# Kernel optimization log

Measured on AMD Instinct MI355X. Metric: run time of the kernel, lower is better.

The kernel has to match this reference:

```python
import jax, jax.numpy as jnp
import numpy as np

B = 1024        # graphs per batch
NPG = 64        # nodes per graph (uniform)
DEG = 16        # avg degree
NE_PG = 256     # candidate non-edges per graph
N = B * NPG
E = N * DEG
NE = B * NE_PG
EMB, HID, NCAT, NET, NOUT = 64, 128, 100, 4, 101  # NOUT = num_external + 1


def setup_inputs() -> dict:
    key = jax.random.key(0)
    ks = jax.random.split(key, 32)
    rn = lambda k, shape: jax.random.normal(k, shape, jnp.float32) * 0.05
    # graph structure: edges and non-edges stay within each graph's node block
    x = jax.random.randint(ks[0], (N,), 0, NCAT)
    offs = jnp.repeat(jnp.arange(B) * NPG, NPG * DEG)
    src = jax.random.randint(ks[1], (E,), 0, NPG) + offs
    dst = jax.random.randint(ks[2], (E,), 0, NPG) + offs
    edge_index = jnp.stack([src, dst])
    edge_attr = jax.random.randint(ks[3], (E,), 0, NET)
    offs_ne = jnp.repeat(jnp.arange(B) * NPG, NE_PG)
    non_edges = jax.random.randint(ks[4], (NE, 2), 0, NPG) + offs_ne[:, None]
    batch = jnp.repeat(jnp.arange(B), NPG)
    return dict(
        node_tab=rn(ks[5], (NCAT, EMB)), edge_tab=rn(ks[6], (NET, EMB)),
        c1_w=rn(ks[7], (EMB, HID)), c1_we=rn(ks[8], (EMB, HID)),
        c1_as=rn(ks[9], (HID,)), c1_ad=rn(ks[10], (HID,)), c1_ae=rn(ks[11], (HID,)), c1_b=rn(ks[12], (HID,)),
        c2_w=rn(ks[13], (HID, HID)), c2_we=rn(ks[14], (EMB, HID)),
        c2_as=rn(ks[15], (HID,)), c2_ad=rn(ks[16], (HID,)), c2_ae=rn(ks[17], (HID,)), c2_b=rn(ks[18], (HID,)),
        s_w1=rn(ks[19], (HID, HID)), s_b1=rn(ks[20], (HID,)), s_w2=rn(ks[21], (HID, 1)), s_b2=rn(ks[22], (1,)),
        n_w1=rn(ks[23], (HID, HID)), n_b1=rn(ks[24], (HID,)), n_w2=rn(ks[25], (HID, NOUT)), n_b2=rn(ks[26], (NOUT,)),
        e_w1=rn(ks[27], (HID, HID)), e_b1=rn(ks[28], (HID,)), e_w2=rn(ks[29], (HID, 1)), e_b2=rn(ks[30], (1,)),
        x=x, edge_index=edge_index, edge_attr=edge_attr, non_edges=non_edges, batch=batch,
    )


def _gat(h_in, src, dst, e, W, We, a_s, a_d, a_e, b):
    """PyG GATConv, heads=1: gather -> leakyrelu logits -> segment softmax over dst -> scatter sum."""
    n = h_in.shape[0]
    h = h_in @ W                  # [N, C]
    he = e @ We                   # [E, C]
    logit = (h @ a_s)[src] + (h @ a_d)[dst] + he @ a_e   # [E]
    logit = jnp.where(logit > 0, logit, 0.2 * logit)      # leaky_relu(0.2)
    m = jax.ops.segment_max(logit, dst, num_segments=n)
    ex = jnp.exp(logit - m[dst])
    den = jax.ops.segment_sum(ex, dst, num_segments=n)
    alpha = ex / (den[dst] + 1e-16)
    return jax.ops.segment_sum(h[src] * alpha[:, None], dst, num_segments=n) + b


def _mlp(z, w1, b1, w2, b2):
    return jax.nn.relu(z @ w1 + b1) @ w2 + b2


def reference(node_tab, edge_tab,
              c1_w, c1_we, c1_as, c1_ad, c1_ae, c1_b,
              c2_w, c2_we, c2_as, c2_ad, c2_ae, c2_b,
              s_w1, s_b1, s_w2, s_b2,
              n_w1, n_b1, n_w2, n_b2,
              e_w1, e_b1, e_w2, e_b2,
              x, edge_index, edge_attr, non_edges, batch):
    src, dst = edge_index[0], edge_index[1]
    e = edge_tab[edge_attr]                      # [E, EMB]
    h = node_tab[x]                              # [N, EMB]
    h = jax.nn.relu(_gat(h, src, dst, e, c1_w, c1_we, c1_as, c1_ad, c1_ae, c1_b))
    h = _gat(h, src, dst, e, c2_w, c2_we, c2_as, c2_ad, c2_ae, c2_b)   # [N, HID]
    g = jax.ops.segment_sum(h, batch, num_segments=B)                   # [B, HID]
    stop = _mlp(g, s_w1, s_b1, s_w2, s_b2)                              # [B, 1]
    addnode = _mlp(h, n_w1, n_b1, n_w2, n_b2)                           # [N, NOUT]
    pair = h[non_edges[:, 0]] + h[non_edges[:, 1]]                      # [NE, HID]
    addedge = _mlp(pair, e_w1, e_b1, e_w2, e_b2)                        # [NE, 1]
    # uniform per-graph sizes -> the torch split/pad is a static reshape+concat
    return jnp.concatenate(
        [stop, addnode.reshape(B, NPG * NOUT), addedge.reshape(B, NE_PG)], axis=1)
```

## Files before the change

kernel.cpp:

```cpp
#include <hip/hip_runtime.h>


#define NPG 64
#define EPG 1024
#define NEPG 256
#define B_GR 1024
#define E_TOT 1048576
#define EMB 64
#define HID 128
#define NOUT 101
#define OUT_PG 6721

typedef __attribute__((ext_vector_type(8))) short bf16x8;
typedef __attribute__((ext_vector_type(4))) float f32x4;
typedef unsigned short ushort_t;

__device__ ushort_t g_c1w[EMB*HID];
__device__ ushort_t g_c2w[HID*HID];
__device__ ushort_t g_nw1[HID*HID];
__device__ ushort_t g_ew1[HID*HID];
__device__ ushort_t g_nw2[HID*112];
__device__ float    g_sw1t[HID*HID];
__device__ float    g_he1[4], g_he2[4];

__device__ __forceinline__ ushort_t f2bf(float f) {
  unsigned u = __float_as_uint(f);
  return (ushort_t)((u + 0x7fffu + ((u >> 16) & 1u)) >> 16);
}
__device__ __forceinline__ float bf2f(ushort_t h) {
  return __uint_as_float(((unsigned)h) << 16);
}

__global__ void prep_kernel(
    const float* __restrict__ edge_tab,
    const float* __restrict__ c1_w,  const float* __restrict__ c1_we,
    const float* __restrict__ c1_ae,
    const float* __restrict__ c2_w,  const float* __restrict__ c2_we,
    const float* __restrict__ c2_ae,
    const float* __restrict__ s_w1,  const float* __restrict__ n_w1,
    const float* __restrict__ n_w2,  const float* __restrict__ e_w1)
{
  const int b = blockIdx.x, tid = threadIdx.x;
  if (b == 0) {
    __shared__ float v1[EMB], v2[EMB];
    if (tid < EMB) {
      float a = 0.f, d = 0.f;
      for (int j = 0; j < HID; ++j) {
        a = fmaf(c1_we[tid*HID + j], c1_ae[j], a);
        d = fmaf(c2_we[tid*HID + j], c2_ae[j], d);
      }
      v1[tid] = a; v2[tid] = d;
    }
    __syncthreads();
    if (tid < 4) {
      float a = 0.f, d = 0.f;
      for (int k = 0; k < EMB; ++k) {
        const float ev = edge_tab[tid*EMB + k];
        a = fmaf(ev, v1[k], a); d = fmaf(ev, v2[k], d);
      }
      g_he1[tid] = a; g_he2[tid] = d;
    }
  } else if (b == 1) {
    for (int idx = tid; idx < EMB*HID; idx += 256) {
      const int j = idx & 7, l = (idx >> 3) & 63, r2 = idx >> 9;
      const int ks = r2 & 1, ct = r2 >> 1;
      const int row = ks*32 + (l >> 4)*8 + j;
      const int col = ct*16 + (l & 15);
      g_c1w[idx] = f2bf(c1_w[row*HID + col]);
    }
  } else if (b >= 2 && b <= 4) {
    const float* W = (b == 2) ? c2_w : (b == 3) ? n_w1 : e_w1;
    ushort_t* G = (b == 2) ? g_c2w : (b == 3) ? g_nw1 : g_ew1;
    for (int idx = tid; idx < HID*HID; idx += 256) {
      const int j = idx & 7, l = (idx >> 3) & 63, r2 = idx >> 9;
      const int ks = r2 & 3, ct = r2 >> 2;
      const int row = ks*32 + (l >> 4)*8 + j;
      const int col = ct*16 + (l & 15);
      G[idx] = f2bf(W[row*HID + col]);
    }
  } else if (b == 5) {
    for (int idx = tid; idx < HID*112; idx += 256) {
      const int j = idx & 7, l = (idx >> 3) & 63, r2 = idx >> 9;
      const int ks = r2 & 3, ct = r2 >> 2;
      const int row = ks*32 + (l >> 4)*8 + j;
      const int col = ct*16 + (l & 15);
      g_nw2[idx] = (col < NOUT) ? f2bf(n_w2[row*NOUT + col]) : (ushort_t)0;
    }
  } else {
    for (int idx = tid; idx < HID*HID; idx += 256)
      g_sw1t[idx] = s_w1[(idx & 127)*HID + (idx >> 7)];
  }
}

#define S_HC   0
#define S_R    18432
#define S_PART 35840
#define S_NS   36864
#define S_ND   37120
#define S_GP   37376
#define S_ZH   37888
#define S_HCC  38400
#define S_TOT  38432

__global__ __launch_bounds__(256, 4) void graph_kernel(
    const float* __restrict__ node_tab,
    const float* __restrict__ c1_as, const float* __restrict__ c1_ad,
    const float* __restrict__ c1_b,
    const float* __restrict__ c2_as, const float* __restrict__ c2_ad,
    const float* __restrict__ c2_b,
    const float* __restrict__ s_b1,  const float* __restrict__ s_w2,
    const float* __restrict__ s_b2,
    const float* __restrict__ n_b1,  const float* __restrict__ n_b2,
    const float* __restrict__ e_b1,  const float* __restrict__ e_w2,
    const float* __restrict__ e_b2,
    const int* __restrict__ x,  const int* __restrict__ ei,
    const int* __restrict__ ea, const int* __restrict__ nedg,
    float* __restrict__ out)
{
  const int tid = threadIdx.x;
  const int gid = blockIdx.x;
  const int nb = gid * NPG;
  const int lane = tid & 63;
  const int wv = tid >> 6;
  const int qd = lane >> 4;
  const int cl = lane & 15;
  const int rb = wv * 16;

  __shared__ __align__(16) char smem[S_TOT];
  ushort_t* Hc   = (ushort_t*)(smem + S_HC);
  float*    Pf   = (float*)   (smem + S_R);
  ushort_t* Hr   = (ushort_t*)(smem + S_R);
  float*    part = (float*)   (smem + S_PART);
  float*    ns   = (float*)   (smem + S_NS);
  float*    nd   = (float*)   (smem + S_ND);
  float*    gp   = (float*)   (smem + S_GP);
  float*    zh   = (float*)   (smem + S_ZH);
  float*    hc   = (float*)   (smem + S_HCC);
  ushort_t* a1b  = Hc;

  unsigned er[4];
  #pragma unroll
  for (int i = 0; i < 4; ++i) {
    const int k = tid + 256*i;
    const int s = ei[gid*EPG + k] - nb;
    const int d = ei[E_TOT + gid*EPG + k] - nb;
    const int t = ea[gid*EPG + k];
    er[i] = (unsigned)(s | (d << 6) | (t << 12));
  }
  bf16x8 ea0, ea1;
  {
    const int cat = x[nb + rb + cl];
    const float* src = node_tab + cat*EMB;
    const float4 v0 = *(const float4*)(src + qd*8);
    const float4 v1 = *(const float4*)(src + qd*8 + 4);
    const float4 v2 = *(const float4*)(src + 32 + qd*8);
    const float4 v3 = *(const float4*)(src + 36 + qd*8);
    ea0[0]=f2bf(v0.x); ea0[1]=f2bf(v0.y); ea0[2]=f2bf(v0.z); ea0[3]=f2bf(v0.w);
    ea0[4]=f2bf(v1.x); ea0[5]=f2bf(v1.y); ea0[6]=f2bf(v1.z); ea0[7]=f2bf(v1.w);
    ea1[0]=f2bf(v2.x); ea1[1]=f2bf(v2.y); ea1[2]=f2bf(v2.z); ea1[3]=f2bf(v2.w);
    ea1[4]=f2bf(v3.x); ea1[5]=f2bf(v3.y); ea1[6]=f2bf(v3.z); ea1[7]=f2bf(v3.w);
  }
  {
    float4* pz = (float4*)Pf;
    #pragma unroll
    for (int j = 0; j < 4; ++j) pz[tid + j*256] = make_float4(0.f,0.f,0.f,0.f);
  }
  if (tid < 128) gp[tid] = 0.f;
  if (tid < 8) hc[tid] = (tid < 4) ? g_he1[tid] : g_he2[tid-4];

  {
    float pns[4] = {0.f,0.f,0.f,0.f}, pnd[4] = {0.f,0.f,0.f,0.f};
    #pragma unroll
    for (int ct = 0; ct < 8; ++ct) {
      f32x4 acc = {0.f, 0.f, 0.f, 0.f};
      const bf16x8 b0 = *(const bf16x8*)(g_c1w + ((ct*2+0)*64 + lane)*8);
      const bf16x8 b1 = *(const bf16x8*)(g_c1w + ((ct*2+1)*64 + lane)*8);
      acc = __builtin_amdgcn_mfma_f32_16x16x32_bf16(ea0, b0, acc, 0, 0, 0);
      acc = __builtin_amdgcn_mfma_f32_16x16x32_bf16(ea1, b1, acc, 0, 0, 0);
      const int n = ct*16 + cl;
      const float asv = c1_as[n], adv = c1_ad[n];
      #pragma unroll
      for (int r = 0; r < 4; ++r) {
        const float v = acc[r];
        Hc[n*72 + (rb + qd*4 + r)] = f2bf(v);
        pns[r] = fmaf(v, asv, pns[r]);
        pnd[r] = fmaf(v, adv, pnd[r]);
      }
    }
    #pragma unroll
    for (int r = 0; r < 4; ++r) {
      #pragma unroll
      for (int off = 1; off < 16; off <<= 1) {
        pns[r] += __shfl_xor(pns[r], off, 64);
        pnd[r] += __shfl_xor(pnd[r], off, 64);
      }
    }
    if (cl == 0) {
      #pragma unroll
      for (int r = 0; r < 4; ++r) { ns[rb+qd*4+r] = pns[r]; nd[rb+qd*4+r] = pnd[r]; }
    }
  }
  __syncthreads();

  #pragma unroll
  for (int i = 0; i < 4; ++i) {
    const unsigned tp = er[i];
    const int s = tp & 63, d = (tp >> 6) & 63, t = tp >> 12;
    float l = ns[s] + nd[d] + hc[t];
    l = (l > 0.f) ? l : 0.2f * l;
    atomicAdd(&Pf[d*64 + s], __expf(l));
  }
  __syncthreads();

  bf16x8 pa0, pa1;
  float inv4[4];
  {
    const float* pr = Pf + (rb + cl)*64;
    const float4 v0 = *(const float4*)(pr + qd*8);
    const float4 v1 = *(const float4*)(pr + qd*8 + 4);
    const float4 v2 = *(const float4*)(pr + 32 + qd*8);
    const float4 v3 = *(const float4*)(pr + 36 + qd*8);
    pa0[0]=f2bf(v0.x); pa0[1]=f2bf(v0.y); pa0[2]=f2bf(v0.z); pa0[3]=f2bf(v0.w);
    pa0[4]=f2bf(v1.x); pa0[5]=f2bf(v1.y); pa0[6]=f2bf(v1.z); pa0[7]=f2bf(v1.w);
    pa1[0]=f2bf(v2.x); pa1[1]=f2bf(v2.y); pa1[2]=f2bf(v2.z); pa1[3]=f2bf(v2.w);
    pa1[4]=f2bf(v3.x); pa1[5]=f2bf(v3.y); pa1[6]=f2bf(v3.z); pa1[7]=f2bf(v3.w);
    float den = v0.x+v0.y+v0.z+v0.w + v1.x+v1.y+v1.z+v1.w
              + v2.x+v2.y+v2.z+v2.w + v3.x+v3.y+v3.z+v3.w;
    den += __shfl_xor(den, 16, 64);
    den += __shfl_xor(den, 32, 64);
    #pragma unroll
    for (int r = 0; r < 4; ++r)
      inv4[r] = 1.f / (__shfl(den, qd*4 + r, 64) + 1e-16f);
  }
  __syncthreads();

  {
    #pragma unroll
    for (int ct = 0; ct < 8; ++ct) {
      f32x4 acc = {0.f, 0.f, 0.f, 0.f};
      const bf16x8 b0 = *(const bf16x8*)(Hc + (ct*16+cl)*72 + qd*8);
      const bf16x8 b1 = *(const bf16x8*)(Hc + (ct*16+cl)*72 + 32 + qd*8);
      acc = __builtin_amdgcn_mfma_f32_16x16x32_bf16(pa0, b0, acc, 0, 0, 0);
      acc = __builtin_amdgcn_mfma_f32_16x16x32_bf16(pa1, b1, acc, 0, 0, 0);
      const int n = ct*16 + cl;
      const float bias = c1_b[n];
      #pragma unroll
      for (int r = 0; r < 4; ++r)
        Hr[(rb + qd*4 + r)*136 + n] = f2bf(fmaxf(fmaf(acc[r], inv4[r], bias), 0.f));
    }
  }
  bf16x8 h1f[4];
  #pragma unroll
  for (int ks = 0; ks < 4; ++ks)
    h1f[ks] = *(const bf16x8*)(Hr + (rb+cl)*136 + ks*32 + qd*8);
  __syncthreads();

  {
    float4* pz = (float4*)Pf;
    #pragma unroll
    for (int j = 0; j < 4; ++j) pz[tid + j*256] = make_float4(0.f,0.f,0.f,0.f);
    float pns[4] = {0.f,0.f,0.f,0.f}, pnd[4] = {0.f,0.f,0.f,0.f};
    #pragma unroll
    for (int ct = 0; ct < 8; ++ct) {
      f32x4 acc = {0.f, 0.f, 0.f, 0.f};
      #pragma unroll
      for (int ks = 0; ks < 4; ++ks) {
        const bf16x8 b = *(const bf16x8*)(g_c2w + ((ct*4+ks)*64 + lane)*8);
        acc = __builtin_amdgcn_mfma_f32_16x16x32_bf16(h1f[ks], b, acc, 0, 0, 0);
      }
      const int n = ct*16 + cl;
      const float asv = c2_as[n], adv = c2_ad[n];
      #pragma unroll
      for (int r = 0; r < 4; ++r) {
        const float v = acc[r];
        Hc[n*72 + (rb + qd*4 + r)] = f2bf(v);
        pns[r] = fmaf(v, asv, pns[r]);
        pnd[r] = fmaf(v, adv, pnd[r]);
      }
    }
    #pragma unroll
    for (int r = 0; r < 4; ++r) {
      #pragma unroll
      for (int off = 1; off < 16; off <<= 1) {
        pns[r] += __shfl_xor(pns[r], off, 64);
        pnd[r] += __shfl_xor(pnd[r], off, 64);
      }
    }
    if (cl == 0) {
      #pragma unroll
      for (int r = 0; r < 4; ++r) { ns[rb+qd*4+r] = pns[r]; nd[rb+qd*4+r] = pnd[r]; }
    }
  }
  __syncthreads();

  #pragma unroll
  for (int i = 0; i < 4; ++i) {
    const unsigned tp = er[i];
    const int s = tp & 63, d = (tp >> 6) & 63, t = tp >> 12;
    float l = ns[s] + nd[d] + hc[4 + t];
    l = (l > 0.f) ? l : 0.2f * l;
    atomicAdd(&Pf[d*64 + s], __expf(l));
  }
  __syncthreads();

  {
    const float* pr = Pf + (rb + cl)*64;
    const float4 v0 = *(const float4*)(pr + qd*8);
    const float4 v1 = *(const float4*)(pr + qd*8 + 4);
    const float4 v2 = *(const float4*)(pr + 32 + qd*8);
    const float4 v3 = *(const float4*)(pr + 36 + qd*8);
    pa0[0]=f2bf(v0.x); pa0[1]=f2bf(v0.y); pa0[2]=f2bf(v0.z); pa0[3]=f2bf(v0.w);
    pa0[4]=f2bf(v1.x); pa0[5]=f2bf(v1.y); pa0[6]=f2bf(v1.z); pa0[7]=f2bf(v1.w);
    pa1[0]=f2bf(v2.x); pa1[1]=f2bf(v2.y); pa1[2]=f2bf(v2.z); pa1[3]=f2bf(v2.w);
    pa1[4]=f2bf(v3.x); pa1[5]=f2bf(v3.y); pa1[6]=f2bf(v3.z); pa1[7]=f2bf(v3.w);
    float den = v0.x+v0.y+v0.z+v0.w + v1.x+v1.y+v1.z+v1.w
              + v2.x+v2.y+v2.z+v2.w + v3.x+v3.y+v3.z+v3.w;
    den += __shfl_xor(den, 16, 64);
    den += __shfl_xor(den, 32, 64);
    #pragma unroll
    for (int r = 0; r < 4; ++r)
      inv4[r] = 1.f / (__shfl(den, qd*4 + r, 64) + 1e-16f);
  }
  __syncthreads();

  {
    #pragma unroll
    for (int ct = 0; ct < 8; ++ct) {
      f32x4 acc = {0.f, 0.f, 0.f, 0.f};
      const bf16x8 b0 = *(const bf16x8*)(Hc + (ct*16+cl)*72 + qd*8);
      const bf16x8 b1 = *(const bf16x8*)(Hc + (ct*16+cl)*72 + 32 + qd*8);
      acc = __builtin_amdgcn_mfma_f32_16x16x32_bf16(pa0, b0, acc, 0, 0, 0);
      acc = __builtin_amdgcn_mfma_f32_16x16x32_bf16(pa1, b1, acc, 0, 0, 0);
      const int n = ct*16 + cl;
      const float bias = c2_b[n];
      float colsum = 0.f;
      #pragma unroll
      for (int r = 0; r < 4; ++r) {
        const float v = fmaf(acc[r], inv4[r], bias);
        Hr[(rb + qd*4 + r)*136 + n] = f2bf(v);
        colsum += v;
      }
      colsum += __shfl_xor(colsum, 16, 64);
      colsum += __shfl_xor(colsum, 32, 64);
      if (qd == 0) atomicAdd(&gp[n], colsum);
    }
  }
  __syncthreads();

  {
    const int j = tid & 127, half = tid >> 7;
    const float* wr = g_sw1t + j*HID + half*64;
    const float* gr = gp + half*64;
    float p = 0.f;
    #pragma unroll
    for (int q = 0; q < 16; ++q) {
      const float4 w = ((const float4*)wr)[q];
      const float4 g = ((const float4*)gr)[q];
      p = fmaf(w.x, g.x, p); p = fmaf(w.y, g.y, p);
      p = fmaf(w.z, g.z, p); p = fmaf(w.w, g.w, p);
    }
    part[tid] = p;
  }
  __syncthreads();
  if (tid < HID) zh[tid] = fmaxf(part[tid] + part[tid+128] + s_b1[tid], 0.f);
  __syncthreads();

  if (tid < 64) {
    float p = fmaf(zh[tid], s_w2[tid], zh[tid+64]*s_w2[tid+64]);
    #pragma unroll
    for (int off = 32; off > 0; off >>= 1) p += __shfl_down(p, off, 64);
    if (tid == 0) out[(size_t)gid*OUT_PG] = p + s_b2[0];
  }
  part[tid] = (tid < 128) ? e_b1[tid] : e_w2[tid-128];

  bf16x8 h2f[4];
  #pragma unroll
  for (int ks = 0; ks < 4; ++ks)
    h2f[ks] = *(const bf16x8*)(Hr + (rb+cl)*136 + ks*32 + qd*8);

  {
    #pragma unroll
    for (int ct = 0; ct < 8; ++ct) {
      f32x4 acc = {0.f, 0.f, 0.f, 0.f};
      #pragma unroll
      for (int ks = 0; ks < 4; ++ks) {
        const bf16x8 b = *(const bf16x8*)(g_nw1 + ((ct*4+ks)*64 + lane)*8);
        acc = __builtin_amdgcn_mfma_f32_16x16x32_bf16(h2f[ks], b, acc, 0, 0, 0);
      }
      const int n = ct*16 + cl;
      const float bias = n_b1[n];
      #pragma unroll
      for (int r = 0; r < 4; ++r)
        a1b[(rb + qd*4 + r)*136 + n] = f2bf(fmaxf(acc[r] + bias, 0.f));
    }
  }
  {
    bf16x8 af[4];
    #pragma unroll
    for (int ks = 0; ks < 4; ++ks)
      af[ks] = *(const bf16x8*)(a1b + (rb+cl)*136 + ks*32 + qd*8);
    float* ob = out + (size_t)gid*OUT_PG + 1;
    #pragma unroll
    for (int ct = 0; ct < 7; ++ct) {
      f32x4 acc = {0.f, 0.f, 0.f, 0.f};
      #pragma unroll
      for (int ks = 0; ks < 4; ++ks) {
        const bf16x8 b = *(const bf16x8*)(g_nw2 + ((ct*4+ks)*64 + lane)*8);
        acc = __builtin_amdgcn_mfma_f32_16x16x32_bf16(af[ks], b, acc, 0, 0, 0);
      }
      const int o = ct*16 + cl;
      if (o < NOUT) {
        const float b2 = n_b2[o];
        #pragma unroll
        for (int r = 0; r < 4; ++r)
          ob[(size_t)(rb + qd*4 + r)*NOUT + o] = acc[r] + b2;
      }
    }
  }
  {
    #pragma unroll
    for (int ct = 0; ct < 8; ++ct) {
      f32x4 acc = {0.f, 0.f, 0.f, 0.f};
      #pragma unroll
      for (int ks = 0; ks < 4; ++ks) {
        const bf16x8 b = *(const bf16x8*)(g_ew1 + ((ct*4+ks)*64 + lane)*8);
        acc = __builtin_amdgcn_mfma_f32_16x16x32_bf16(h2f[ks], b, acc, 0, 0, 0);
      }
      const int n = ct*16 + cl;
      #pragma unroll
      for (int r = 0; r < 4; ++r)
        a1b[(rb + qd*4 + r)*136 + n] = f2bf(acc[r]);
    }
  }
  __syncthreads();

  {
    const int2 pr = *(const int2*)(nedg + 2*(gid*NEPG + tid));
    const ushort_t* ui = a1b + (pr.x - nb)*136;
    const ushort_t* uj = a1b + (pr.y - nb)*136;
    float ssum = 0.f;
    #pragma unroll
    for (int q8 = 0; q8 < 16; ++q8) {
      const bf16x8 va = *(const bf16x8*)(ui + q8*8);
      const bf16x8 vb = *(const bf16x8*)(uj + q8*8);
      #pragma unroll
      for (int j = 0; j < 8; ++j) {
        const int c = q8*8 + j;
        float v = bf2f((ushort_t)va[j]) + bf2f((ushort_t)vb[j]) + part[c];
        v = fmaxf(v, 0.f);
        ssum = fmaf(v, part[128 + c], ssum);
      }
    }
    out[(size_t)gid*OUT_PG + 1 + NPG*NOUT + tid] = ssum + e_b2[0];
  }
}

extern "C" void kernel_launch(void* const* d_in, const int* in_sizes, int n_in,
                              void* d_out, int out_size, void* d_ws, size_t ws_size,
                              hipStream_t stream) {
  const float* node_tab = (const float*)d_in[0];
  const float* edge_tab = (const float*)d_in[1];
  const float* c1_w  = (const float*)d_in[2];
  const float* c1_we = (const float*)d_in[3];
  const float* c1_as = (const float*)d_in[4];
  const float* c1_ad = (const float*)d_in[5];
  const float* c1_ae = (const float*)d_in[6];
  const float* c1_b  = (const float*)d_in[7];
  const float* c2_w  = (const float*)d_in[8];
  const float* c2_we = (const float*)d_in[9];
  const float* c2_as = (const float*)d_in[10];
  const float* c2_ad = (const float*)d_in[11];
  const float* c2_ae = (const float*)d_in[12];
  const float* c2_b  = (const float*)d_in[13];
  const float* s_w1  = (const float*)d_in[14];
  const float* s_b1  = (const float*)d_in[15];
  const float* s_w2  = (const float*)d_in[16];
  const float* s_b2  = (const float*)d_in[17];
  const float* n_w1  = (const float*)d_in[18];
  const float* n_b1  = (const float*)d_in[19];
  const float* n_w2  = (const float*)d_in[20];
  const float* n_b2  = (const float*)d_in[21];
  const float* e_w1  = (const float*)d_in[22];
  const float* e_b1  = (const float*)d_in[23];
  const float* e_w2  = (const float*)d_in[24];
  const float* e_b2  = (const float*)d_in[25];
  const int* x    = (const int*)d_in[26];
  const int* ei   = (const int*)d_in[27];
  const int* ea   = (const int*)d_in[28];
  const int* nedg = (const int*)d_in[29];
  float* out = (float*)d_out;

  prep_kernel<<<dim3(7), dim3(256), 0, stream>>>(
      edge_tab, c1_w, c1_we, c1_ae, c2_w, c2_we, c2_ae,
      s_w1, n_w1, n_w2, e_w1);

  graph_kernel<<<dim3(B_GR), dim3(256), 0, stream>>>(
      node_tab, c1_as, c1_ad, c1_b, c2_as, c2_ad, c2_b,
      s_b1, s_w2, s_b2, n_b1, n_b2, e_b1, e_w2, e_b2,
      x, ei, ea, nedg, out);
}
```

Measured before the change: 201.6 us.

## Parallelize weight prep across more blocks and fuse node/edge MLP first layers

The prep kernel is split from 7 blocks into 44, so each block converts a 2048-element chunk of the weights. In the graph kernel, the node-MLP and edge-MLP first-layer MFMA loops now share the loaded h2 fragments and run interleaved. The edge projection is written into the Hr region, which removes one barrier and the separate pass. The edge bias/weight vector gets its own shared-memory slot, the stop-head hidden computation is inlined to drop a sync, and the non-edge index load is hoisted to kernel start. The cost is more live registers in the fused loop and slightly more shared memory.

New measurement: 190.5 us. -5.5%, faster.

```diff
diff --git a/kernel.cpp b/kernel.cpp
--- a/kernel.cpp
+++ b/kernel.cpp
@@ -60,35 +60,58 @@
       }
       g_he1[tid] = a; g_he2[tid] = d;
     }
-  } else if (b == 1) {
-    for (int idx = tid; idx < EMB*HID; idx += 256) {
+    return;
+  }
+  if (b <= 4) {
+    const int base = (b - 1) * 2048 + tid;
+    #pragma unroll
+    for (int it = 0; it < 8; ++it) {
+      const int idx = base + it*256;
       const int j = idx & 7, l = (idx >> 3) & 63, r2 = idx >> 9;
       const int ks = r2 & 1, ct = r2 >> 1;
       const int row = ks*32 + (l >> 4)*8 + j;
       const int col = ct*16 + (l & 15);
       g_c1w[idx] = f2bf(c1_w[row*HID + col]);
     }
-  } else if (b >= 2 && b <= 4) {
-    const float* W = (b == 2) ? c2_w : (b == 3) ? n_w1 : e_w1;
-    ushort_t* G = (b == 2) ? g_c2w : (b == 3) ? g_nw1 : g_ew1;
-    for (int idx = tid; idx < HID*HID; idx += 256) {
+    return;
+  }
+  if (b <= 28) {
+    const int grp = (b - 5) >> 3;
+    const int chunk = (b - 5) & 7;
+    const float* W = (grp == 0) ? c2_w : (grp == 1) ? n_w1 : e_w1;
+    ushort_t* G = (grp == 0) ? g_c2w : (grp == 1) ? g_nw1 : g_ew1;
+    const int base = chunk * 2048 + tid;
+    #pragma unroll
+    for (int it = 0; it < 8; ++it) {
+      const int idx = base + it*256;
       const int j = idx & 7, l = (idx >> 3) & 63, r2 = idx >> 9;
       const int ks = r2 & 3, ct = r2 >> 2;
       const int row = ks*32 + (l >> 4)*8 + j;
       const int col = ct*16 + (l & 15);
       G[idx] = f2bf(W[row*HID + col]);
     }
-  } else if (b == 5) {
-    for (int idx = tid; idx < HID*112; idx += 256) {
+    return;
+  }
+  if (b <= 35) {
+    const int base = (b - 29) * 2048 + tid;
+    #pragma unroll
+    for (int it = 0; it < 8; ++it) {
+      const int idx = base + it*256;
       const int j = idx & 7, l = (idx >> 3) & 63, r2 = idx >> 9;
       const int ks = r2 & 3, ct = r2 >> 2;
       const int row = ks*32 + (l >> 4)*8 + j;
       const int col = ct*16 + (l & 15);
       g_nw2[idx] = (col < NOUT) ? f2bf(n_w2[row*NOUT + col]) : (ushort_t)0;
     }
-  } else {
-    for (int idx = tid; idx < HID*HID; idx += 256)
+    return;
+  }
+  {
+    const int base = (b - 36) * 2048 + tid;
+    #pragma unroll
+    for (int it = 0; it < 8; ++it) {
+      const int idx = base + it*256;
       g_sw1t[idx] = s_w1[(idx & 127)*HID + (idx >> 7)];
+    }
   }
 }
 
@@ -98,9 +121,9 @@
 #define S_NS   36864
 #define S_ND   37120
 #define S_GP   37376
-#define S_ZH   37888
-#define S_HCC  38400
-#define S_TOT  38432
+#define S_EBW  37888
+#define S_HCC  38912
+#define S_TOT  38944
 
 __global__ __launch_bounds__(256, 4) void graph_kernel(
     const float* __restrict__ node_tab,
@@ -134,7 +157,7 @@
   float*    ns   = (float*)   (smem + S_NS);
   float*    nd   = (float*)   (smem + S_ND);
   float*    gp   = (float*)   (smem + S_GP);
-  float*    zh   = (float*)   (smem + S_ZH);
+  float*    ebw  = (float*)   (smem + S_EBW);
   float*    hc   = (float*)   (smem + S_HCC);
   ushort_t* a1b  = Hc;
 
@@ -147,6 +170,7 @@
     const int t = ea[gid*EPG + k];
     er[i] = (unsigned)(s | (d << 6) | (t << 12));
   }
+  const int2 prr = *(const int2*)(nedg + 2*(gid*NEPG + tid));
   bf16x8 ea0, ea1;
   {
     const int cat = x[nb + rb + cl];
@@ -166,6 +190,7 @@
     for (int j = 0; j < 4; ++j) pz[tid + j*256] = make_float4(0.f,0.f,0.f,0.f);
   }
   if (tid < 128) gp[tid] = 0.f;
+  ebw[tid] = (tid < 128) ? e_b1[tid] : e_w2[tid - 128];
   if (tid < 8) hc[tid] = (tid < 4) ? g_he1[tid] : g_he2[tid-4];
 
   {
@@ -362,16 +387,15 @@
     part[tid] = p;
   }
   __syncthreads();
-  if (tid < HID) zh[tid] = fmaxf(part[tid] + part[tid+128] + s_b1[tid], 0.f);
-  __syncthreads();
 
   if (tid < 64) {
-    float p = fmaf(zh[tid], s_w2[tid], zh[tid+64]*s_w2[tid+64]);
+    const float z0 = fmaxf(part[tid] + part[tid+128] + s_b1[tid], 0.f);
+    const float z1 = fmaxf(part[tid+64] + part[tid+192] + s_b1[tid+64], 0.f);
+    float p = fmaf(z0, s_w2[tid], z1 * s_w2[tid+64]);
     #pragma unroll
     for (int off = 32; off > 0; off >>= 1) p += __shfl_down(p, off, 64);
     if (tid == 0) out[(size_t)gid*OUT_PG] = p + s_b2[0];
   }
-  part[tid] = (tid < 128) ? e_b1[tid] : e_w2[tid-128];
 
   bf16x8 h2f[4];
   #pragma unroll
@@ -381,17 +405,22 @@
   {
     #pragma unroll
     for (int ct = 0; ct < 8; ++ct) {
-      f32x4 acc = {0.f, 0.f, 0.f, 0.f};
+      f32x4 an = {0.f, 0.f, 0.f, 0.f};
+      f32x4 ae2 = {0.f, 0.f, 0.f, 0.f};
       #pragma unroll
       for (int ks = 0; ks < 4; ++ks) {
-        const bf16x8 b = *(const bf16x8*)(g_nw1 + ((ct*4+ks)*64 + lane)*8);
-        acc = __builtin_amdgcn_mfma_f32_16x16x32_bf16(h2f[ks], b, acc, 0, 0, 0);
+        const bf16x8 bn = *(const bf16x8*)(g_nw1 + ((ct*4+ks)*64 + lane)*8);
+        const bf16x8 be = *(const bf16x8*)(g_ew1 + ((ct*4+ks)*64 + lane)*8);
+        an  = __builtin_amdgcn_mfma_f32_16x16x32_bf16(h2f[ks], bn, an, 0, 0, 0);
+        ae2 = __builtin_amdgcn_mfma_f32_16x16x32_bf16(h2f[ks], be, ae2, 0, 0, 0);
       }
       const int n = ct*16 + cl;
       const float bias = n_b1[n];
       #pragma unroll
-      for (int r = 0; r < 4; ++r)
-        a1b[(rb + qd*4 + r)*136 + n] = f2bf(fmaxf(acc[r] + bias, 0.f));
+      for (int r = 0; r < 4; ++r) {
+        a1b[(rb + qd*4 + r)*136 + n] = f2bf(fmaxf(an[r] + bias, 0.f));
+        Hr[(rb + qd*4 + r)*136 + n] = f2bf(ae2[r]);
+      }
     }
   }
   {
@@ -417,27 +446,11 @@
       }
     }
   }
-  {
-    #pragma unroll
-    for (int ct = 0; ct < 8; ++ct) {
-      f32x4 acc = {0.f, 0.f, 0.f, 0.f};
-      #pragma unroll
-      for (int ks = 0; ks < 4; ++ks) {
-        const bf16x8 b = *(const bf16x8*)(g_ew1 + ((ct*4+ks)*64 + lane)*8);
-        acc = __builtin_amdgcn_mfma_f32_16x16x32_bf16(h2f[ks], b, acc, 0, 0, 0);
-      }
-      const int n = ct*16 + cl;
-      #pragma unroll
-      for (int r = 0; r < 4; ++r)
-        a1b[(rb + qd*4 + r)*136 + n] = f2bf(acc[r]);
-    }
-  }
-  __syncthreads();
-
-  {
-    const int2 pr = *(const int2*)(nedg + 2*(gid*NEPG + tid));
-    const ushort_t* ui = a1b + (pr.x - nb)*136;
-    const ushort_t* uj = a1b + (pr.y - nb)*136;
+  __syncthreads();
+
+  {
+    const ushort_t* ui = Hr + (prr.x - nb)*136;
+    const ushort_t* uj = Hr + (prr.y - nb)*136;
     float ssum = 0.f;
     #pragma unroll
     for (int q8 = 0; q8 < 16; ++q8) {
@@ -446,9 +459,9 @@
       #pragma unroll
       for (int j = 0; j < 8; ++j) {
         const int c = q8*8 + j;
-        float v = bf2f((ushort_t)va[j]) + bf2f((ushort_t)vb[j]) + part[c];
+        float v = bf2f((ushort_t)va[j]) + bf2f((ushort_t)vb[j]) + ebw[c];
         v = fmaxf(v, 0.f);
-        ssum = fmaf(v, part[128 + c], ssum);
+        ssum = fmaf(v, ebw[128 + c], ssum);
       }
     }
     out[(size_t)gid*OUT_PG + 1 + NPG*NOUT + tid] = ssum + e_b2[0];
@@ -490,7 +503,7 @@
   const int* nedg = (const int*)d_in[29];
   float* out = (float*)d_out;
 
-  prep_kernel<<<dim3(7), dim3(256), 0, stream>>>(
+  prep_kernel<<<dim3(44), dim3(256), 0, stream>>>(
       edge_tab, c1_w, c1_we, c1_ae, c2_w, c2_we, c2_ae,
       s_w1, n_w1, n_w2, e_w1);
 
```
